# Kernel tuning notes

Hardware: AMD Instinct MI355X
Metric: run time of the kernel (lower is better)

## Reference

```python
import jax, jax.numpy as jnp
import numpy as np
from jax import lax

B, C, H, W = 16, 256, 56, 56
GROUPS = 4
K = 3
DILATIONS = (1, 3, 5)
EPS = 1e-5


@jax.custom_vjp
def bin_act(x):
    return jnp.sign(x)

def _bin_act_fwd(x):
    return jnp.sign(x), x

def _bin_act_bwd(x, g):
    grad = jnp.where((x >= -1.0) & (x <= 0.0), 2.0 + 2.0 * x, 0.0) \
         + jnp.where((x > 0.0) & (x <= 1.0), 2.0 - 2.0 * x, 0.0)
    return (grad * g,)

bin_act.defvjp(_bin_act_fwd, _bin_act_bwd)


def _bin_weight(wi):
    # per-output-channel scaling from raw |w|, centered sign, clip-STE
    scale = lax.stop_gradient(jnp.mean(jnp.abs(wi), axis=(1, 2, 3), keepdims=True))
    wc = wi - jnp.mean(wi, axis=(1, 2, 3), keepdims=True)
    clipped = jnp.clip(wc, -1.0, 1.0)
    return lax.stop_gradient(scale * jnp.sign(wc) - clipped) + clipped


def setup_inputs() -> dict:
    key = jax.random.key(0)
    ks = jax.random.split(key, 3)
    x = jax.random.normal(ks[0], (B, C, H, W), dtype=jnp.float32)
    # 3 branches of grouped conv weights: (3, C_out, C_in/groups, K, K)
    w = jax.random.normal(ks[1], (3, C, C // GROUPS, K, K), dtype=jnp.float32) * 0.05
    cb = jax.random.normal(ks[2], (3, C), dtype=jnp.float32) * 0.01
    return {
        "x": x,
        "bias": jnp.zeros((1, C, 1, 1), jnp.float32),   # LearnableBias
        "w": w,
        "cb": cb,                                        # conv biases
        "move1": jnp.zeros((3, C), jnp.float32),
        "alpha": jnp.full((3, C), 0.25, jnp.float32),    # PReLU slopes
        "move2": jnp.zeros((3, C), jnp.float32),
        "gamma": jnp.ones((C,), jnp.float32),            # LayerNorm weight
        "beta": jnp.zeros((C,), jnp.float32),            # LayerNorm bias
    }


def reference(x, bias, w, cb, move1, alpha, move2, gamma, beta):
    xb = x + bias
    xq = bin_act(xb)  # binarized activations, shared across branches
    out = jnp.zeros_like(x)
    for i, d in enumerate(DILATIONS):
        wq = _bin_weight(w[i])
        y = lax.conv_general_dilated(
            xq, wq,
            window_strides=(1, 1),
            padding=[(d, d), (d, d)],  # 'same' for k=3 with dilation d
            rhs_dilation=(d, d),
            dimension_numbers=("NCHW", "OIHW", "NCHW"),
            feature_group_count=GROUPS,
        )
        y = y + cb[i][None, :, None, None]
        # RPReLU: shift, channel-wise PReLU, shift
        y = y - move1[i][None, :, None, None]
        y = jnp.where(y >= 0, y, alpha[i][None, :, None, None] * y)
        y = y + move2[i][None, :, None, None]
        out = out + y
    # LayerNorm over channel dim (equivalent to NHWC last-dim LN)
    mean = jnp.mean(out, axis=1, keepdims=True)
    var = jnp.var(out, axis=1, keepdims=True)
    out = (out - mean) * lax.rsqrt(var + EPS)
    out = out * gamma[None, :, None, None] + beta[None, :, None, None]
    return out
```

## Files before the change

### kernel.cpp

```cpp
#include <hip/hip_runtime.h>
#include <hip/hip_fp16.h>
#include <stdint.h>

static constexpr int Bc = 16, Cc = 256, Hc = 56, Wc = 56, Gc = 4;
static constexpr int HWc = Hc * Wc;
static constexpr float EPSc = 1e-5f;
static constexpr int ROWP = 72;
static constexpr int COL0 = 8;


__global__ __launch_bounds__(256) void k_prep(
    const float* __restrict__ w, const float* __restrict__ x,
    const float* __restrict__ bias, uint64_t* __restrict__ wbits,
    float* __restrict__ scales, uint64_t* __restrict__ abits,
    uint32_t* __restrict__ zero_area) {
  const int t = threadIdx.x;
  if (blockIdx.x < 192) {
    const int io = blockIdx.x * 4 + (t >> 6);
    const int i = io >> 8, o = io & 255;
    const int lane = t & 63;
    const float* wp = w + (size_t)io * 576 + lane * 9;
    float v[9];
    float ssum = 0.f, sabs = 0.f;
#pragma unroll
    for (int k = 0; k < 9; ++k) {
      v[k] = wp[k];
      ssum += v[k];
      sabs += fabsf(v[k]);
    }
#pragma unroll
    for (int off = 32; off > 0; off >>= 1) {
      ssum += __shfl_down(ssum, off);
      sabs += __shfl_down(sabs, off);
    }
    const float mean = __shfl(ssum, 0) * (1.f / 576.f);
    const float scale = __shfl(sabs, 0) * (1.f / 576.f);
#pragma unroll
    for (int k = 0; k < 9; ++k) {
      unsigned long long m = __ballot(v[k] > mean);
      if (lane == 0) wbits[(i * 9 + k) * Cc + o] = m;
    }
    if (lane == 0) scales[io] = scale;
  } else if (blockIdx.x == 192) {
    zero_area[t] = 0;
  } else {
    const int bid = blockIdx.x - 193;
    const int b = bid / Hc, h = bid % Hc;
    const int g = t >> 6, lane = t & 63;
    const float* xp = x + ((size_t)(b * Cc + g * 64 + lane)) * HWc + h * Wc;
    const float bc = bias[g * 64 + lane];
    uint64_t* rowp = abits + (((size_t)b * Gc + g) * Hc + h) * ROWP;
    if (lane < COL0) {
      rowp[lane] = 0;
      rowp[COL0 + Wc + lane] = 0;
    }
#pragma unroll
    for (int k = 0; k < 14; ++k) {
      const float4 v = *(const float4*)(xp + k * 4);
      const unsigned long long m0 = __ballot(v.x + bc > 0.f);
      const unsigned long long m1 = __ballot(v.y + bc > 0.f);
      const unsigned long long m2 = __ballot(v.z + bc > 0.f);
      const unsigned long long m3 = __ballot(v.w + bc > 0.f);
      if (lane == 0) {
        ulonglong2 s01, s23;
        s01.x = m0; s01.y = m1;
        s23.x = m2; s23.y = m3;
        *(ulonglong2*)(rowp + COL0 + 4 * k) = s01;
        *(ulonglong2*)(rowp + COL0 + 4 * k + 2) = s23;
      }
    }
  }
}

template <int D>
struct Branch {
  uint64_t wgt[9];
  const uint64_t *r0, *r1, *r2;
  int BM, ZL, ZR;
  float sc, cbm1, al;

  __device__ __forceinline__ void init(const uint64_t* __restrict__ wb,
                                       const uint64_t* rowbase,
                                       const uint64_t* zrowp, int h,
                                       float sc_, float cbm1_, float al_) {
    sc = sc_; cbm1 = cbm1_; al = al_;
    int z[9];
#pragma unroll
    for (int k = 0; k < 9; ++k) {
      wgt[k] = wb[k * Cc];
      z[k] = 64 - 2 * (int)__builtin_popcountll(wgt[k]);
    }
    const bool v0 = (h - D >= 0), v2 = (h + D < Hc);
    r0 = v0 ? (rowbase + (size_t)(h - D) * ROWP) : zrowp;
    r1 = rowbase + (size_t)h * ROWP;
    r2 = v2 ? (rowbase + (size_t)(h + D) * ROWP) : zrowp;
    const int Zrow = (v0 ? 0 : (z[0] + z[1] + z[2])) +
                     (v2 ? 0 : (z[6] + z[7] + z[8]));
    BM = 576 - Zrow;
    ZL = (v0 ? z[0] : 0) + z[3] + (v2 ? z[6] : 0);
    ZR = (v0 ? z[2] : 0) + z[5] + (v2 ? z[8] : 0);
  }

  template <int N>
  __device__ __forceinline__ void accum(int w0, int acc[N]) const {
#pragma unroll
    for (int kh = 0; kh < 3; ++kh) {
      const uint64_t* rp = (kh == 0) ? r0 : (kh == 1 ? r1 : r2);
      uint64_t seg[N + 2 * D];
#pragma unroll
      for (int j = 0; j < N + 2 * D; ++j) seg[j] = rp[w0 - D + j];
#pragma unroll
      for (int ww = 0; ww < N; ++ww) {
#pragma unroll
        for (int kw = 0; kw < 3; ++kw)
          acc[ww] +=
              (int)__builtin_popcountll(wgt[kh * 3 + kw] ^ seg[ww + D * kw]);
      }
    }
  }

  template <int N>
  __device__ __forceinline__ void epi(int w0, const int acc[N],
                                      float outf[N]) const {
#pragma unroll
    for (int ww = 0; ww < N; ++ww) {
      const int w = w0 + ww;
      const int B = BM - ((w < D) ? ZL : 0) - ((w >= Wc - D) ? ZR : 0);
      const float y0 = fmaf(sc, (float)(B - 2 * acc[ww]), cbm1);
      outf[ww] += fmaxf(y0, 0.f) + al * fminf(y0, 0.f);
    }
  }
};

static constexpr int WH = 28;
static constexpr int TSH = 30;
static constexpr int NCH = 7;

__global__ __launch_bounds__(256, 4) void k_conv_ln(
    const uint64_t* __restrict__ abits, const uint64_t* __restrict__ zrowp,
    const uint64_t* __restrict__ wbits, const float* __restrict__ scales,
    const float* __restrict__ cb, const float* __restrict__ mv1,
    const float* __restrict__ al, const float* __restrict__ mv2,
    const float* __restrict__ gamma, const float* __restrict__ beta,
    float* __restrict__ out) {
  __shared__ __half out_tile[Cc * TSH];
  __shared__ float redu[4][WH], redq[4][WH];
  __shared__ float mstat[WH], rstat[WH];

  const int wh = blockIdx.x & 1;
  const int bh = blockIdx.x >> 1;
  const int b = bh / Hc, h = bh % Hc;
  const int W0 = wh * WH;
  const int t = threadIdx.x;
  const int gu = __builtin_amdgcn_readfirstlane(t >> 6);

  const uint64_t* rowbase = abits + ((size_t)b * Gc + gu) * Hc * ROWP + COL0;

  Branch<1> b0; Branch<3> b1; Branch<5> b2;
  b0.init(wbits + 0 * 9 * Cc + t, rowbase, zrowp, h, scales[0 * Cc + t],
          cb[0 * Cc + t] - mv1[0 * Cc + t], al[0 * Cc + t]);
  b1.init(wbits + 1 * 9 * Cc + t, rowbase, zrowp, h, scales[1 * Cc + t],
          cb[1 * Cc + t] - mv1[1 * Cc + t], al[1 * Cc + t]);
  b2.init(wbits + 2 * 9 * Cc + t, rowbase, zrowp, h, scales[2 * Cc + t],
          cb[2 * Cc + t] - mv1[2 * Cc + t], al[2 * Cc + t]);
  const float m2sum = mv2[0 * Cc + t] + mv2[1 * Cc + t] + mv2[2 * Cc + t];

#pragma unroll 1
  for (int ch = 0; ch < 4; ++ch) {
    const int w0 = W0 + ch * NCH;
    float outf[NCH];
#pragma unroll
    for (int ww = 0; ww < NCH; ++ww) outf[ww] = m2sum;
    { int acc[NCH] = {}; b0.accum<NCH>(w0, acc); b0.epi<NCH>(w0, acc, outf); }
    { int acc[NCH] = {}; b1.accum<NCH>(w0, acc); b1.epi<NCH>(w0, acc, outf); }
    { int acc[NCH] = {}; b2.accum<NCH>(w0, acc); b2.epi<NCH>(w0, acc, outf); }
#pragma unroll
    for (int ww = 0; ww < NCH; ++ww)
      out_tile[t * TSH + ch * NCH + ww] = __float2half(outf[ww]);
  }
  __syncthreads();

  if (t < 4 * WH) {
    const int ww = t % WH;
    const int cq = t / WH;
    float s = 0.f, sq = 0.f;
#pragma unroll 4
    for (int c = cq * 64; c < cq * 64 + 64; ++c) {
      const float v = __half2float(out_tile[c * TSH + ww]);
      s += v;
      sq = fmaf(v, v, sq);
    }
    redu[cq][ww] = s;
    redq[cq][ww] = sq;
  }
  __syncthreads();
  if (t < WH) {
    const float s = redu[0][t] + redu[1][t] + redu[2][t] + redu[3][t];
    const float sq = redq[0][t] + redq[1][t] + redq[2][t] + redq[3][t];
    const float mean = s * (1.f / 256.f);
    const float var = sq * (1.f / 256.f) - mean * mean;
    mstat[t] = mean;
    rstat[t] = rsqrtf(var + EPSc);
  }
  __syncthreads();

  float* base = out + ((size_t)b * Cc * Hc + h) * Wc + W0;
  for (int idx = t; idx < Cc * WH; idx += 256) {
    const int c = idx / WH;
    const int ww = idx - c * WH;
    const float v = __half2float(out_tile[c * TSH + ww]);
    base[(size_t)c * HWc + ww] = (v - mstat[ww]) * rstat[ww] * gamma[c] + beta[c];
  }
}

extern "C" void kernel_launch(void* const* d_in, const int* in_sizes, int n_in,
                              void* d_out, int out_size, void* d_ws, size_t ws_size,
                              hipStream_t stream) {
  const float* x     = (const float*)d_in[0];
  const float* bias  = (const float*)d_in[1];
  const float* w     = (const float*)d_in[2];
  const float* cb    = (const float*)d_in[3];
  const float* mv1   = (const float*)d_in[4];
  const float* al    = (const float*)d_in[5];
  const float* mv2   = (const float*)d_in[6];
  const float* gamma = (const float*)d_in[7];
  const float* beta  = (const float*)d_in[8];
  float* out = (float*)d_out;

  uint8_t* ws = (uint8_t*)d_ws;
  uint32_t* zero_area = (uint32_t*)ws;
  const uint64_t* zrowp = (const uint64_t*)ws + COL0;
  uint64_t* abits = (uint64_t*)(ws + 1024);
  const size_t abits_bytes = (size_t)Bc * Gc * Hc * ROWP * 8;
  uint64_t* wbits = (uint64_t*)(ws + 1024 + abits_bytes);
  float* scales = (float*)(ws + 1024 + abits_bytes + 6912 * 8);

  hipLaunchKernelGGL(k_prep, dim3(192 + 1 + Bc * Hc), dim3(256), 0, stream,
                     w, x, bias, wbits, scales, abits, zero_area);
  hipLaunchKernelGGL(k_conv_ln, dim3(Bc * Hc * 2), dim3(256), 0, stream,
                     abits, zrowp, wbits, scales, cb, mv1, al, mv2, gamma, beta,
                     out);
}
```

Baseline: 193.4 us.

## Coalesce activation binarization via LDS transpose and share center-row loads across branches

The prep kernel now binarizes activations with each block covering half the channels of one row. Threads issue coalesced float4 loads across channels, write sign bytes into shared memory, then pack them into 64-bit words. This replaces the per-channel strided loads and per-lane ballots, at the cost of doubling the grid and adding a shared-memory transpose. The conv kernel loads the center row once per chunk and reuses it for all three dilation branches, and interior chunks use a simplified epilogue without border corrections.

Result: faster. 180.1 us (-6.9%).

```diff
diff --git a/kernel.cpp b/kernel.cpp
--- a/kernel.cpp
+++ b/kernel.cpp
@@ -8,6 +8,8 @@
 static constexpr int ROWP = 72;
 static constexpr int COL0 = 8;
 
+
+static constexpr int SBS2 = 132;
 
 __global__ __launch_bounds__(256) void k_prep(
     const float* __restrict__ w, const float* __restrict__ x,
@@ -44,38 +46,53 @@
   } else if (blockIdx.x == 192) {
     zero_area[t] = 0;
   } else {
+    __shared__ uint8_t sb[Wc * SBS2];
     const int bid = blockIdx.x - 193;
-    const int b = bid / Hc, h = bid % Hc;
-    const int g = t >> 6, lane = t & 63;
-    const float* xp = x + ((size_t)(b * Cc + g * 64 + lane)) * HWc + h * Wc;
-    const float bc = bias[g * 64 + lane];
-    uint64_t* rowp = abits + (((size_t)b * Gc + g) * Hc + h) * ROWP;
-    if (lane < COL0) {
-      rowp[lane] = 0;
-      rowp[COL0 + Wc + lane] = 0;
-    }
-#pragma unroll
-    for (int k = 0; k < 14; ++k) {
-      const float4 v = *(const float4*)(xp + k * 4);
-      const unsigned long long m0 = __ballot(v.x + bc > 0.f);
-      const unsigned long long m1 = __ballot(v.y + bc > 0.f);
-      const unsigned long long m2 = __ballot(v.z + bc > 0.f);
-      const unsigned long long m3 = __ballot(v.w + bc > 0.f);
-      if (lane == 0) {
-        ulonglong2 s01, s23;
-        s01.x = m0; s01.y = m1;
-        s23.x = m2; s23.y = m3;
-        *(ulonglong2*)(rowp + COL0 + 4 * k) = s01;
-        *(ulonglong2*)(rowp + COL0 + 4 * k + 2) = s23;
+    const int b = bid / 112;
+    const int rem = bid - b * 112;
+    const int h = rem >> 1, chh = rem & 1;
+    const float* xb = x + ((size_t)(b * Cc + chh * 128)) * HWc + h * Wc;
+#pragma unroll
+    for (int k = 0; k < 7; ++k) {
+      const int idx = k * 256 + t;
+      const int cl = idx / 14, q = idx - cl * 14;
+      const float4 v = *(const float4*)(xb + (size_t)cl * HWc + q * 4);
+      const float bc = bias[chh * 128 + cl];
+      sb[(q * 4 + 0) * SBS2 + cl] = (v.x + bc > 0.f);
+      sb[(q * 4 + 1) * SBS2 + cl] = (v.y + bc > 0.f);
+      sb[(q * 4 + 2) * SBS2 + cl] = (v.z + bc > 0.f);
+      sb[(q * 4 + 3) * SBS2 + cl] = (v.w + bc > 0.f);
+    }
+    __syncthreads();
+    if (t < 2 * ROWP) {
+      const int gl = t / ROWP, k = t - gl * ROWP;
+      uint64_t word = 0;
+      if (k >= COL0 && k < COL0 + Wc) {
+        const int ww = k - COL0;
+        const uint32_t* p = (const uint32_t*)(sb + ww * SBS2 + gl * 64);
+        uint64_t acc = 0;
+#pragma unroll
+        for (int dw = 0; dw < 16; ++dw) {
+          const uint32_t d = p[dw];
+          const uint32_t nib = (d | (d >> 7) | (d >> 14) | (d >> 21)) & 0xF;
+          acc |= (uint64_t)nib << (4 * dw);
+        }
+        word = acc;
       }
+      const int g = chh * 2 + gl;
+      abits[(((size_t)b * Gc + g) * Hc + h) * ROWP + k] = word;
     }
   }
 }
+
+static constexpr int NCH = 7;
+static constexpr int WH = 28;
+static constexpr int TSH = 30;
 
 template <int D>
 struct Branch {
   uint64_t wgt[9];
-  const uint64_t *r0, *r1, *r2;
+  const uint64_t *r0, *r2;
   int BM, ZL, ZR;
   float sc, cbm1, al;
 
@@ -92,7 +109,6 @@
     }
     const bool v0 = (h - D >= 0), v2 = (h + D < Hc);
     r0 = v0 ? (rowbase + (size_t)(h - D) * ROWP) : zrowp;
-    r1 = rowbase + (size_t)h * ROWP;
     r2 = v2 ? (rowbase + (size_t)(h + D) * ROWP) : zrowp;
     const int Zrow = (v0 ? 0 : (z[0] + z[1] + z[2])) +
                      (v2 ? 0 : (z[6] + z[7] + z[8]));
@@ -101,16 +117,15 @@
     ZR = (v0 ? z[2] : 0) + z[5] + (v2 ? z[8] : 0);
   }
 
-  template <int N>
-  __device__ __forceinline__ void accum(int w0, int acc[N]) const {
-#pragma unroll
-    for (int kh = 0; kh < 3; ++kh) {
-      const uint64_t* rp = (kh == 0) ? r0 : (kh == 1 ? r1 : r2);
-      uint64_t seg[N + 2 * D];
-#pragma unroll
-      for (int j = 0; j < N + 2 * D; ++j) seg[j] = rp[w0 - D + j];
-#pragma unroll
-      for (int ww = 0; ww < N; ++ww) {
+  __device__ __forceinline__ void accum_edge(int w0, int acc[NCH]) const {
+#pragma unroll
+    for (int kh = 0; kh < 3; kh += 2) {
+      const uint64_t* rp = (kh == 0) ? r0 : r2;
+      uint64_t seg[NCH + 2 * D];
+#pragma unroll
+      for (int j = 0; j < NCH + 2 * D; ++j) seg[j] = rp[w0 - D + j];
+#pragma unroll
+      for (int ww = 0; ww < NCH; ++ww) {
 #pragma unroll
         for (int kw = 0; kw < 3; ++kw)
           acc[ww] +=
@@ -119,11 +134,30 @@
     }
   }
 
-  template <int N>
-  __device__ __forceinline__ void epi(int w0, const int acc[N],
-                                      float outf[N]) const {
-#pragma unroll
-    for (int ww = 0; ww < N; ++ww) {
+  __device__ __forceinline__ void accum_mid(const uint64_t* smid,
+                                            int acc[NCH]) const {
+#pragma unroll
+    for (int ww = 0; ww < NCH; ++ww) {
+#pragma unroll
+      for (int kw = 0; kw < 3; ++kw)
+        acc[ww] += (int)__builtin_popcountll(
+            wgt[3 + kw] ^ smid[ww + 5 - D + D * kw]);
+    }
+  }
+
+  __device__ __forceinline__ void epi_int(const int acc[NCH],
+                                          float outf[NCH]) const {
+#pragma unroll
+    for (int ww = 0; ww < NCH; ++ww) {
+      const float y0 = fmaf(sc, (float)(BM - 2 * acc[ww]), cbm1);
+      outf[ww] += fmaxf(y0, 0.f) + al * fminf(y0, 0.f);
+    }
+  }
+
+  __device__ __forceinline__ void epi_edge(int w0, const int acc[NCH],
+                                           float outf[NCH]) const {
+#pragma unroll
+    for (int ww = 0; ww < NCH; ++ww) {
       const int w = w0 + ww;
       const int B = BM - ((w < D) ? ZL : 0) - ((w >= Wc - D) ? ZR : 0);
       const float y0 = fmaf(sc, (float)(B - 2 * acc[ww]), cbm1);
@@ -131,10 +165,6 @@
     }
   }
 };
-
-static constexpr int WH = 28;
-static constexpr int TSH = 30;
-static constexpr int NCH = 7;
 
 __global__ __launch_bounds__(256, 4) void k_conv_ln(
     const uint64_t* __restrict__ abits, const uint64_t* __restrict__ zrowp,
@@ -155,6 +185,7 @@
   const int gu = __builtin_amdgcn_readfirstlane(t >> 6);
 
   const uint64_t* rowbase = abits + ((size_t)b * Gc + gu) * Hc * ROWP + COL0;
+  const uint64_t* r1 = rowbase + (size_t)h * ROWP;
 
   Branch<1> b0; Branch<3> b1; Branch<5> b2;
   b0.init(wbits + 0 * 9 * Cc + t, rowbase, zrowp, h, scales[0 * Cc + t],
@@ -168,12 +199,28 @@
 #pragma unroll 1
   for (int ch = 0; ch < 4; ++ch) {
     const int w0 = W0 + ch * NCH;
+    uint64_t smid[17];
+#pragma unroll
+    for (int j = 0; j < 17; ++j) smid[j] = r1[w0 - 5 + j];
+    const bool interior = (w0 >= 5) && (w0 <= Wc - NCH - 5);
     float outf[NCH];
 #pragma unroll
     for (int ww = 0; ww < NCH; ++ww) outf[ww] = m2sum;
-    { int acc[NCH] = {}; b0.accum<NCH>(w0, acc); b0.epi<NCH>(w0, acc, outf); }
-    { int acc[NCH] = {}; b1.accum<NCH>(w0, acc); b1.epi<NCH>(w0, acc, outf); }
-    { int acc[NCH] = {}; b2.accum<NCH>(w0, acc); b2.epi<NCH>(w0, acc, outf); }
+    {
+      int acc[NCH] = {};
+      b0.accum_edge(w0, acc); b0.accum_mid(smid, acc);
+      if (interior) b0.epi_int(acc, outf); else b0.epi_edge(w0, acc, outf);
+    }
+    {
+      int acc[NCH] = {};
+      b1.accum_edge(w0, acc); b1.accum_mid(smid, acc);
+      if (interior) b1.epi_int(acc, outf); else b1.epi_edge(w0, acc, outf);
+    }
+    {
+      int acc[NCH] = {};
+      b2.accum_edge(w0, acc); b2.accum_mid(smid, acc);
+      if (interior) b2.epi_int(acc, outf); else b2.epi_edge(w0, acc, outf);
+    }
 #pragma unroll
     for (int ww = 0; ww < NCH; ++ww)
       out_tile[t * TSH + ch * NCH + ww] = __float2half(outf[ww]);
@@ -235,7 +282,7 @@
   uint64_t* wbits = (uint64_t*)(ws + 1024 + abits_bytes);
   float* scales = (float*)(ws + 1024 + abits_bytes + 6912 * 8);
 
-  hipLaunchKernelGGL(k_prep, dim3(192 + 1 + Bc * Hc), dim3(256), 0, stream,
+  hipLaunchKernelGGL(k_prep, dim3(192 + 1 + Bc * Hc * 2), dim3(256), 0, stream,
                      w, x, bias, wbits, scales, abits, zero_area);
   hipLaunchKernelGGL(k_conv_ln, dim3(Bc * Hc * 2), dim3(256), 0, stream,
                      abits, zrowp, wbits, scales, cb, mv1, al, mv2, gamma, beta,
```
